# Optimization experiments

Measured on AMD Instinct MI355X. Metric: run time of the kernel, lower is better.

Reference implementation:

```python
import jax, jax.numpy as jnp
import numpy as np

HIDDEN = 1024
N_HEADS = 16
HEAD_DIM = HIDDEN // N_HEADS


def _rope_tables(seq_len, dim, dtype):
    inv_freq = 1.0 / (10000.0 ** (jnp.arange(0, dim, 2, dtype=jnp.float32) / dim))
    t = jnp.arange(seq_len, dtype=jnp.float32)
    freqs = jnp.einsum('i,j->ij', t, inv_freq)          # [S, dim/2]
    emb = jnp.concatenate([freqs, freqs], axis=-1)       # [S, dim]
    cos = jnp.cos(emb)[None, :, None, :].astype(dtype)   # [1, S, 1, dim]
    sin = jnp.sin(emb)[None, :, None, :].astype(dtype)
    return cos, sin


def _rotate_half(x):
    x1, x2 = x[..., : x.shape[-1] // 2], x[..., x.shape[-1] // 2 :]
    return jnp.concatenate([-x2, x1], axis=-1)


def setup_inputs() -> dict:
    key = jax.random.key(0)
    ks = jax.random.split(key, 9)
    s = 1.0 / np.sqrt(HIDDEN)
    return {
        'x': jax.random.normal(ks[0], (2, 2048, HIDDEN), dtype=jnp.float32),
        'q_w': jax.random.uniform(ks[1], (HIDDEN, HIDDEN), jnp.float32, -s, s),
        'q_b': jax.random.uniform(ks[2], (HIDDEN,), jnp.float32, -s, s),
        'k_w': jax.random.uniform(ks[3], (HIDDEN, HIDDEN), jnp.float32, -s, s),
        'k_b': jax.random.uniform(ks[4], (HIDDEN,), jnp.float32, -s, s),
        'v_w': jax.random.uniform(ks[5], (HIDDEN, HIDDEN), jnp.float32, -s, s),
        'v_b': jax.random.uniform(ks[6], (HIDDEN,), jnp.float32, -s, s),
        'o_w': jax.random.uniform(ks[7], (HIDDEN, HIDDEN), jnp.float32, -s, s),
        'o_b': jax.random.uniform(ks[8], (HIDDEN,), jnp.float32, -s, s),
    }


def reference(x, q_w, q_b, k_w, k_b, v_w, v_b, o_w, o_b):
    B, S, _ = x.shape
    scale = HEAD_DIM ** -0.5
    # projections (torch Linear: x @ W.T + b)
    q = (x @ q_w.T + q_b).reshape(B, S, N_HEADS, HEAD_DIM)
    k = (x @ k_w.T + k_b).reshape(B, S, N_HEADS, HEAD_DIM)
    v = (x @ v_w.T + v_b).reshape(B, S, N_HEADS, HEAD_DIM)
    # RoPE
    cos, sin = _rope_tables(S, HEAD_DIM, x.dtype)
    q = q * cos + _rotate_half(q) * sin
    k = k * cos + _rotate_half(k) * sin
    # attention: [B, H, S, S]
    scores = jnp.einsum('bqhd,bkhd->bhqk', q, k) * scale
    attn = jax.nn.softmax(scores, axis=-1)
    out = jnp.einsum('bhqk,bkhd->bqhd', attn, v).reshape(B, S, HIDDEN)
    return out @ o_w.T + o_b
```

## Files before the change

kernel.cpp:

```cpp
#include <hip/hip_runtime.h>
#include <hip/hip_bf16.h>


#define SEQ    2048
#define BATCH  2
#define NHEADS 16
#define HDIM   64
#define HID    1024
#define NTOK   (BATCH*SEQ)

typedef __bf16 bf16x8 __attribute__((ext_vector_type(8)));
typedef float  f32x4  __attribute__((ext_vector_type(4)));
typedef unsigned short u16x8 __attribute__((ext_vector_type(8)));

__device__ __forceinline__ unsigned short bfc(float x) {
  return __builtin_bit_cast(unsigned short, (__bf16)x);
}
#define EXP2(x) __builtin_amdgcn_exp2f(x)

__device__ __forceinline__ void gload16(const void* gptr, void* ldsptr) {
  typedef __attribute__((address_space(3))) unsigned int as3_uint;
  typedef const __attribute__((address_space(1))) unsigned int as1_uint;
  __builtin_amdgcn_global_load_lds(
      (as1_uint*)(unsigned long long)gptr,
      (as3_uint*)(unsigned int)(unsigned long long)ldsptr,
      16, 0, 0);
}

__device__ __forceinline__ void cvt8(const float* __restrict__ s,
                                     unsigned short* __restrict__ d, int i) {
  float4 a = *reinterpret_cast<const float4*>(s + i);
  float4 b = *reinterpret_cast<const float4*>(s + i + 4);
  u16x8 o;
  o[0] = bfc(a.x); o[1] = bfc(a.y); o[2] = bfc(a.z); o[3] = bfc(a.w);
  o[4] = bfc(b.x); o[5] = bfc(b.y); o[6] = bfc(b.z); o[7] = bfc(b.w);
  *reinterpret_cast<u16x8*>(d + i) = o;
}

__global__ __launch_bounds__(256) void prep(
    const float* __restrict__ x,
    const float* __restrict__ qw, const float* __restrict__ kw,
    const float* __restrict__ vw, const float* __restrict__ ow,
    unsigned short* __restrict__ xb,
    unsigned short* __restrict__ wqb, unsigned short* __restrict__ wkb,
    unsigned short* __restrict__ wvb, unsigned short* __restrict__ wob,
    float* __restrict__ ct, float* __restrict__ st)
{
  const int XN = NTOK * HID / 8;
  const int WN = HID * HID / 8;
  int tid = blockIdx.x * 256 + threadIdx.x;
  if (tid < XN) {
    cvt8(x, xb, tid * 8);
  } else if (tid < XN + 4 * WN) {
    int r = tid - XN;
    int which = r >> 17;
    int i = (r & (WN - 1)) * 8;
    const float* s = (which == 0) ? qw : (which == 1) ? kw : (which == 2) ? vw : ow;
    unsigned short* d = (which == 0) ? wqb : (which == 1) ? wkb : (which == 2) ? wvb : wob;
    cvt8(s, d, i);
  } else {
    int idx = tid - (XN + 4 * WN);
    if (idx < SEQ * 32) {
      int p = idx >> 5, j = idx & 31;
      float inv = powf(10000.0f, -(float)(2 * j) * (1.0f / 64.0f));
      float a = (float)p * inv;
      ct[idx] = cosf(a);
      st[idx] = sinf(a);
    }
  }
}

__global__ __launch_bounds__(256) void gemm_qkv(
    const unsigned short* __restrict__ X,
    const unsigned short* __restrict__ Wq, const unsigned short* __restrict__ Wk,
    const unsigned short* __restrict__ Wv,
    const float* __restrict__ bq, const float* __restrict__ bk, const float* __restrict__ bv,
    const float* __restrict__ ct, const float* __restrict__ st,
    unsigned short* __restrict__ Qo, unsigned short* __restrict__ Ko,
    unsigned short* __restrict__ VTo)
{
  __shared__ unsigned short LSH[24576];
  const int z = blockIdx.z;
  const unsigned short* W = (z == 0) ? Wq : (z == 1) ? Wk : Wv;
  const float* bias = (z == 0) ? bq : (z == 1) ? bk : bv;
  const int tm = blockIdx.x, tn = blockIdx.y;
  const int t = threadIdx.x, w = t >> 6, l = t & 63;
  const int wm = w >> 1, wn = w & 1, g = l >> 4;

  f32x4 acc[4][4] = {};

  const int arow0 = tm * 128, brow0 = tn * 128;
  const int s0 = w * 2, s1 = w * 2 + 1;
  const int r0 = s0 * 16 + (l >> 2), r1 = s1 * 16 + (l >> 2);
  const int kc = (l & 3) * 8;

#define GSTAGE(buf, k0)                                                               \
  {                                                                                   \
    gload16(X + (long)(arow0 + r0) * HID + (k0) + kc, LSH + (buf) * 4096 + s0 * 512); \
    gload16(X + (long)(arow0 + r1) * HID + (k0) + kc, LSH + (buf) * 4096 + s1 * 512); \
    gload16(W + (long)(brow0 + r0) * HID + (k0) + kc, LSH + 12288 + (buf) * 4096 + s0 * 512); \
    gload16(W + (long)(brow0 + r1) * HID + (k0) + kc, LSH + 12288 + (buf) * 4096 + s1 * 512); \
  }

  GSTAGE(0, 0)
  GSTAGE(1, 32)
  asm volatile("s_waitcnt vmcnt(4)" ::: "memory");
  __builtin_amdgcn_s_barrier();
  int cur = 0, stg = 2;
  for (int k0 = 0; k0 < HID; k0 += 32) {
    if (k0 + 64 < HID) GSTAGE(stg, k0 + 64)
    bf16x8 af[4], bfr[4];
#pragma unroll
    for (int fm = 0; fm < 4; ++fm)
      af[fm] = *reinterpret_cast<const bf16x8*>(
          LSH + cur * 4096 + (wm * 64 + fm * 16 + (l & 15)) * 32 + g * 8);
#pragma unroll
    for (int fn = 0; fn < 4; ++fn)
      bfr[fn] = *reinterpret_cast<const bf16x8*>(
          LSH + 12288 + cur * 4096 + (wn * 64 + fn * 16 + (l & 15)) * 32 + g * 8);
    __builtin_amdgcn_s_setprio(1);
#pragma unroll
    for (int fm = 0; fm < 4; ++fm)
#pragma unroll
      for (int fn = 0; fn < 4; ++fn)
        acc[fm][fn] = __builtin_amdgcn_mfma_f32_16x16x32_bf16(af[fm], bfr[fn], acc[fm][fn], 0, 0, 0);
    __builtin_amdgcn_s_setprio(0);
    if (k0 + 64 < HID) {
      asm volatile("s_waitcnt vmcnt(4)" ::: "memory");
    } else {
      asm volatile("s_waitcnt vmcnt(0)" ::: "memory");
    }
    __builtin_amdgcn_s_barrier();
    cur = (cur == 2) ? 0 : cur + 1;
    stg = (stg == 2) ? 0 : stg + 1;
  }
#undef GSTAGE

  const int colb = brow0 + wn * 64;
  float bsv[4];
#pragma unroll
  for (int fn = 0; fn < 4; ++fn) bsv[fn] = bias[colb + fn * 16 + (l & 15)];

  if (z == 2) {
#pragma unroll
    for (int fm = 0; fm < 4; ++fm) {
      int tok = wm * 64 + fm * 16 + g * 4;
#pragma unroll
      for (int fn = 0; fn < 4; ++fn) {
        int col = wn * 64 + fn * 16 + (l & 15);
        unsigned int u0 = (unsigned int)bfc(acc[fm][fn][0] + bsv[fn]) |
                          ((unsigned int)bfc(acc[fm][fn][1] + bsv[fn]) << 16);
        unsigned int u1 = (unsigned int)bfc(acc[fm][fn][2] + bsv[fn]) |
                          ((unsigned int)bfc(acc[fm][fn][3] + bsv[fn]) << 16);
        uint2 uv; uv.x = u0; uv.y = u1;
        *reinterpret_cast<uint2*>(&LSH[col * 128 + (tok ^ ((col & 7) << 3))]) = uv;
      }
    }
    __syncthreads();
    const int bb = arow0 >> 11, stok = arow0 & (SEQ - 1);
#pragma unroll
    for (int p8 = 0; p8 < 8; ++p8) {
      int col = p8 * 16 + (t >> 4);
      int soff = (t & 15) * 8;
      uint4 v = *reinterpret_cast<const uint4*>(&LSH[col * 128 + (soff ^ ((col & 7) << 3))]);
      int hh = (brow0 + col) >> 6;
      int dd = col & 63;
      unsigned short* dst = VTo + ((long)(bb * NHEADS + hh) * HDIM + dd) * SEQ + stok + soff;
      *reinterpret_cast<uint4*>(dst) = v;
    }
    return;
  }

  unsigned short* Out = (z == 0) ? Qo : Ko;
  const int h = colb >> 6;
#pragma unroll
  for (int fm = 0; fm < 4; ++fm) {
#pragma unroll
    for (int r = 0; r < 4; ++r) {
      int grow = arow0 + wm * 64 + fm * 16 + g * 4 + r;
      int b = grow >> 11, sidx = grow & (SEQ - 1);
      unsigned short* ob = Out + ((long)(b * NHEADS + h) * SEQ + sidx) * HDIM;
#pragma unroll
      for (int fn2 = 0; fn2 < 2; ++fn2) {
        int d1 = fn2 * 16 + (l & 15);
        float v1 = acc[fm][fn2][r] + bsv[fn2];
        float v2 = acc[fm][fn2 + 2][r] + bsv[fn2 + 2];
        float c = ct[sidx * 32 + d1], sn = st[sidx * 32 + d1];
        float o1 = v1 * c - v2 * sn;
        float o2 = v2 * c + v1 * sn;
        if (z == 0) { o1 *= 0.18033688f; o2 *= 0.18033688f; }
        ob[d1] = bfc(o1);
        ob[d1 + 32] = bfc(o2);
      }
    }
  }
}

__global__ __launch_bounds__(256) void attn(
    const unsigned short* __restrict__ Qb,
    const unsigned short* __restrict__ Kb,
    const unsigned short* __restrict__ VTb,
    unsigned short* __restrict__ Ob)
{
  __shared__ unsigned short Kl[2][64 * 64];
  __shared__ unsigned short Vl[4][64 * 64];
  __shared__ unsigned short Pl[4][32 * 64];
  __shared__ unsigned short Vext[16 * 64];
  const int bh = blockIdx.x, qt = blockIdx.y;
  const int b = bh >> 4, h = bh & 15;
  const int t = threadIdx.x, w = t >> 6, l = t & 63;
  const long hb = (long)bh * SEQ * HDIM;
  const int g = l >> 4;
  const int swz = (l & 7) << 4;

  const int q0 = qt * 128 + w * 32;
  bf16x8 qf[2][2];
#pragma unroll
  for (int f = 0; f < 2; ++f)
#pragma unroll
    for (int ks = 0; ks < 2; ++ks)
      qf[f][ks] = *reinterpret_cast<const bf16x8*>(
          Qb + hb + (long)(q0 + f * 16 + (l & 15)) * HDIM + ks * 32 + g * 8);

  f32x4 oacc[2][4] = {};
  f32x4 oaccE[2] = {};
  const f32x4 FZERO = {0.f, 0.f, 0.f, 0.f};

  const int rowq = (l & 15) * 128;
  const int colx0 = (g * 16) ^ swz;
  const int colx1 = (64 + g * 16) ^ swz;
  char* const Pw = (char*)Pl + w * 4096;

  const int srow = l >> 3;
  const int scol = (((l & 7) * 16) ^ ((l >> 3) << 4)) >> 1;
  const unsigned short* kp0 = Kb + hb + (long)(w * 16 + srow) * HDIM + scol;
  const unsigned short* kp1 = kp0 + 8 * HDIM;
  const unsigned short* vp0 = VTb + hb + (long)(w * 16 + srow) * SEQ + scol;
  const unsigned short* vp1 = vp0 + 8 * SEQ;

#define STAGE(kbuf, vbuf)                                              \
  {                                                                    \
    gload16(kp0, (char*)Kl + (kbuf) * 8192 + w * 2048);                \
    gload16(kp1, (char*)Kl + (kbuf) * 8192 + w * 2048 + 1024);         \
    gload16(vp0, (char*)Vl + (vbuf) * 8192 + w * 2048);                \
    gload16(vp1, (char*)Vl + (vbuf) * 8192 + w * 2048 + 1024);         \
    kp0 += 64 * HDIM; kp1 += 64 * HDIM; vp0 += 64; vp1 += 64;          \
  }

#define QK(kbuf)                                                                  \
  _Pragma("unroll")                                                               \
  for (int fnK = 0; fnK < 4; ++fnK) {                                             \
    const char* kb_ = (char*)Kl + (kbuf) * 8192 + fnK * 2048 + rowq;              \
    bf16x8 kf0 = *reinterpret_cast<const bf16x8*>(kb_ + colx0);                   \
    bf16x8 kf1 = *reinterpret_cast<const bf16x8*>(kb_ + colx1);                   \
    sa[0][fnK] = __builtin_amdgcn_mfma_f32_16x16x32_bf16(kf0, qf[0][0], FZERO, 0, 0, 0); \
    sa[0][fnK] = __builtin_amdgcn_mfma_f32_16x16x32_bf16(kf1, qf[0][1], sa[0][fnK], 0, 0, 0); \
    sa[1][fnK] = __builtin_amdgcn_mfma_f32_16x16x32_bf16(kf0, qf[1][0], FZERO, 0, 0, 0); \
    sa[1][fnK] = __builtin_amdgcn_mfma_f32_16x16x32_bf16(kf1, qf[1][1], sa[1][fnK], 0, 0, 0); \
  }

#define PFREAD                                                                    \
  _Pragma("unroll")                                                               \
  for (int f = 0; f < 2; ++f) {                                                   \
    pf[f][0] = *reinterpret_cast<const bf16x8*>(Pw + f * 2048 + rowq + colx0);    \
    pf[f][1] = *reinterpret_cast<const bf16x8*>(Pw + f * 2048 + rowq + colx1);    \
  }

#define PVSTEP(vbuf)                                                              \
  _Pragma("unroll")                                                               \
  for (int fnD = 0; fnD < 4; ++fnD) {                                             \
    const char* vb_ = (char*)Vl + (vbuf) * 8192 + fnD * 2048 + rowq;              \
    bf16x8 vf0 = *reinterpret_cast<const bf16x8*>(vb_ + colx0);                   \
    bf16x8 vf1 = *reinterpret_cast<const bf16x8*>(vb_ + colx1);                   \
    oacc[0][fnD] = __builtin_amdgcn_mfma_f32_16x16x32_bf16(vf0, pf[0][0], oacc[0][fnD], 0, 0, 0); \
    oacc[0][fnD] = __builtin_amdgcn_mfma_f32_16x16x32_bf16(vf1, pf[0][1], oacc[0][fnD], 0, 0, 0); \
    oacc[1][fnD] = __builtin_amdgcn_mfma_f32_16x16x32_bf16(vf0, pf[1][0], oacc[1][fnD], 0, 0, 0); \
    oacc[1][fnD] = __builtin_amdgcn_mfma_f32_16x16x32_bf16(vf1, pf[1][1], oacc[1][fnD], 0, 0, 0); \
  }                                                                               \
  oaccE[0] = __builtin_amdgcn_mfma_f32_16x16x32_bf16(vxf0, pf[0][0], oaccE[0], 0, 0, 0); \
  oaccE[0] = __builtin_amdgcn_mfma_f32_16x16x32_bf16(vxf1, pf[0][1], oaccE[0], 0, 0, 0); \
  oaccE[1] = __builtin_amdgcn_mfma_f32_16x16x32_bf16(vxf0, pf[1][0], oaccE[1], 0, 0, 0); \
  oaccE[1] = __builtin_amdgcn_mfma_f32_16x16x32_bf16(vxf1, pf[1][1], oaccE[1], 0, 0, 0);

#define SOFTPACK                                                                  \
  _Pragma("unroll")                                                               \
  for (int f = 0; f < 2; ++f) {                                                   \
    _Pragma("unroll")                                                             \
    for (int fn = 0; fn < 4; ++fn)                                                \
      _Pragma("unroll")                                                           \
      for (int r = 0; r < 4; ++r) sa[f][fn][r] = EXP2(sa[f][fn][r]);              \
    char* pw_ = Pw + f * 2048 + rowq;                                             \
    _Pragma("unroll")                                                             \
    for (int fn = 0; fn < 4; ++fn) {                                              \
      unsigned int u0 = (unsigned int)bfc(sa[f][fn][0]) | ((unsigned int)bfc(sa[f][fn][1]) << 16); \
      unsigned int u1 = (unsigned int)bfc(sa[f][fn][2]) | ((unsigned int)bfc(sa[f][fn][3]) << 16); \
      uint2 uv; uv.x = u0; uv.y = u1;                                             \
      *reinterpret_cast<uint2*>(pw_ + ((fn * 32 + g * 8) ^ swz)) = uv;            \
    }                                                                             \
  }

#define ITER(KB, VR, VW)                                   \
  {                                                        \
    PFREAD                                                 \
    STAGE(KB ^ 1, VW)                                      \
    __builtin_amdgcn_s_setprio(1);                         \
    QK(KB)                                                 \
    PVSTEP(VR)                                             \
    __builtin_amdgcn_s_setprio(0);                         \
    SOFTPACK                                               \
    asm volatile("s_waitcnt vmcnt(0)" ::: "memory");       \
    __builtin_amdgcn_s_barrier();                          \
  }
#define ITER_NOSTAGE(KB, VR)                               \
  {                                                        \
    PFREAD                                                 \
    __builtin_amdgcn_s_setprio(1);                         \
    QK(KB)                                                 \
    PVSTEP(VR)                                             \
    __builtin_amdgcn_s_setprio(0);                         \
    SOFTPACK                                               \
    asm volatile("s_waitcnt vmcnt(0)" ::: "memory");       \
    __builtin_amdgcn_s_barrier();                          \
  }

  f32x4 sa[2][4];
  bf16x8 pf[2][2];

  {
    int i = t * 4;
#pragma unroll
    for (int j = 0; j < 4; ++j)
      Vext[i + j] = (i + j) < 64 ? (unsigned short)0x3F80 : (unsigned short)0;
  }

  STAGE(0, 0)
  asm volatile("s_waitcnt vmcnt(0)" ::: "memory");
  __builtin_amdgcn_s_barrier();

  const bf16x8 vxf0 = *reinterpret_cast<const bf16x8*>((char*)Vext + rowq + colx0);
  const bf16x8 vxf1 = *reinterpret_cast<const bf16x8*>((char*)Vext + rowq + colx1);

  STAGE(1, 1)
  __builtin_amdgcn_s_setprio(1);
  QK(0)
  __builtin_amdgcn_s_setprio(0);
  SOFTPACK
  asm volatile("s_waitcnt vmcnt(0)" ::: "memory");
  __builtin_amdgcn_s_barrier();

  for (int m = 0; m < 7; ++m) {
    ITER(1, 0, 2)
    ITER(0, 1, 3)
    ITER(1, 2, 0)
    ITER(0, 3, 1)
  }
  ITER(1, 0, 2)
  ITER(0, 1, 3)
  ITER_NOSTAGE(1, 2)

  PFREAD
  __builtin_amdgcn_s_setprio(1);
  PVSTEP(3)
  __builtin_amdgcn_s_setprio(0);

#undef STAGE
#undef QK
#undef PFREAD
#undef PVSTEP
#undef SOFTPACK
#undef ITER
#undef ITER_NOSTAGE

#pragma unroll
  for (int f = 0; f < 2; ++f) {
    float lr = __shfl(oaccE[f][0], l & 15);
    float inv = 1.0f / lr;
    int q = q0 + f * 16 + (l & 15);
    unsigned short* op = Ob + (long)(b * SEQ + q) * HID + h * HDIM;
#pragma unroll
    for (int fnD = 0; fnD < 4; ++fnD) {
      unsigned int lo = (unsigned int)bfc(oacc[f][fnD][0] * inv) |
                        ((unsigned int)bfc(oacc[f][fnD][1] * inv) << 16);
      unsigned int hi = (unsigned int)bfc(oacc[f][fnD][2] * inv) |
                        ((unsigned int)bfc(oacc[f][fnD][3] * inv) << 16);
      uint2 uv; uv.x = lo; uv.y = hi;
      *reinterpret_cast<uint2*>(op + fnD * 16 + g * 4) = uv;
    }
  }
}

__global__ __launch_bounds__(256) void gemm_o(
    const unsigned short* __restrict__ A,
    const unsigned short* __restrict__ W,
    const float* __restrict__ bias,
    float* __restrict__ Out)
{
  __shared__ unsigned short Al[3][128 * 32];
  __shared__ unsigned short Bl[3][64 * 32];
  const int tm = blockIdx.x, tn = blockIdx.y;
  const int t = threadIdx.x, w = t >> 6, l = t & 63;
  const int wm = w >> 1, wn = w & 1;

  f32x4 acc[4][2] = {};
  const int arow0 = tm * 128, brow0 = tn * 64;
  const int s0 = w * 2, s1 = w * 2 + 1;
  const int r0 = s0 * 16 + (l >> 2), r1 = s1 * 16 + (l >> 2);
  const int rb = w * 16 + (l >> 2);
  const int kc = (l & 3) * 8;

#define GSTAGE(buf, k0)                                                       \
  {                                                                           \
    gload16(A + (long)(arow0 + r0) * HID + (k0) + kc, Al[buf] + s0 * 512);    \
    gload16(A + (long)(arow0 + r1) * HID + (k0) + kc, Al[buf] + s1 * 512);    \
    gload16(W + (long)(brow0 + rb) * HID + (k0) + kc, Bl[buf] + w * 512);     \
  }

  GSTAGE(0, 0)
  GSTAGE(1, 32)
  asm volatile("s_waitcnt vmcnt(3)" ::: "memory");
  __builtin_amdgcn_s_barrier();
  int cur = 0, stg = 2;
  for (int k0 = 0; k0 < HID; k0 += 32) {
    if (k0 + 64 < HID) GSTAGE(stg, k0 + 64)
    bf16x8 af[4], bfr[2];
#pragma unroll
    for (int fm = 0; fm < 4; ++fm)
      af[fm] = *reinterpret_cast<const bf16x8*>(Al[cur] + (wm * 64 + fm * 16 + (l & 15)) * 32 + (l >> 4) * 8);
#pragma unroll
    for (int fn = 0; fn < 2; ++fn)
      bfr[fn] = *reinterpret_cast<const bf16x8*>(Bl[cur] + (wn * 32 + fn * 16 + (l & 15)) * 32 + (l >> 4) * 8);
    __builtin_amdgcn_s_setprio(1);
#pragma unroll
    for (int fm = 0; fm < 4; ++fm)
#pragma unroll
      for (int fn = 0; fn < 2; ++fn)
        acc[fm][fn] = __builtin_amdgcn_mfma_f32_16x16x32_bf16(af[fm], bfr[fn], acc[fm][fn], 0, 0, 0);
    __builtin_amdgcn_s_setprio(0);
    if (k0 + 64 < HID) {
      asm volatile("s_waitcnt vmcnt(3)" ::: "memory");
    } else {
      asm volatile("s_waitcnt vmcnt(0)" ::: "memory");
    }
    __builtin_amdgcn_s_barrier();
    cur = (cur == 2) ? 0 : cur + 1;
    stg = (stg == 2) ? 0 : stg + 1;
  }
#undef GSTAGE

  const int colb = brow0 + wn * 32;
  float bsv[2];
#pragma unroll
  for (int fn = 0; fn < 2; ++fn) bsv[fn] = bias[colb + fn * 16 + (l & 15)];
#pragma unroll
  for (int fm = 0; fm < 4; ++fm)
#pragma unroll
    for (int r = 0; r < 4; ++r) {
      int grow = arow0 + wm * 64 + fm * 16 + (l >> 4) * 4 + r;
#pragma unroll
      for (int fn = 0; fn < 2; ++fn)
        Out[(long)grow * HID + colb + fn * 16 + (l & 15)] = acc[fm][fn][r] + bsv[fn];
    }
}

extern "C" void kernel_launch(void* const* d_in, const int* in_sizes, int n_in,
                              void* d_out, int out_size, void* d_ws, size_t ws_size,
                              hipStream_t stream) {
  const float* x  = (const float*)d_in[0];
  const float* qw = (const float*)d_in[1];
  const float* qb = (const float*)d_in[2];
  const float* kw = (const float*)d_in[3];
  const float* kb = (const float*)d_in[4];
  const float* vw = (const float*)d_in[5];
  const float* vb = (const float*)d_in[6];
  const float* ow = (const float*)d_in[7];
  const float* ob = (const float*)d_in[8];
  float* out = (float*)d_out;

  char* p = (char*)d_ws;
  unsigned short* xb  = (unsigned short*)p; p += (size_t)NTOK * HID * 2;
  unsigned short* wqb = (unsigned short*)p; p += (size_t)HID * HID * 2;
  unsigned short* wkb = (unsigned short*)p; p += (size_t)HID * HID * 2;
  unsigned short* wvb = (unsigned short*)p; p += (size_t)HID * HID * 2;
  unsigned short* wob = (unsigned short*)p; p += (size_t)HID * HID * 2;
  unsigned short* Qb  = (unsigned short*)p; p += (size_t)NTOK * HID * 2;
  unsigned short* Kb  = (unsigned short*)p; p += (size_t)NTOK * HID * 2;
  unsigned short* VTb = (unsigned short*)p; p += (size_t)NTOK * HID * 2;
  float* ct = (float*)p; p += (size_t)SEQ * 32 * 4;
  float* st = (float*)p; p += (size_t)SEQ * 32 * 4;
  unsigned short* Ab  = xb;

  const int XN = NTOK * HID / 8, WN = HID * HID / 8;
  const int prep_threads = XN + 4 * WN + SEQ * 32;
  prep<<<dim3((prep_threads + 255) / 256), 256, 0, stream>>>(
      x, qw, kw, vw, ow, xb, wqb, wkb, wvb, wob, ct, st);

  gemm_qkv<<<dim3(NTOK / 128, HID / 128, 3), 256, 0, stream>>>(
      xb, wqb, wkb, wvb, qb, kb, vb, ct, st, Qb, Kb, VTb);

  attn<<<dim3(BATCH * NHEADS, SEQ / 128), 256, 0, stream>>>(Qb, Kb, VTb, Ab);

  gemm_o<<<dim3(NTOK / 128, HID / 64), 256, 0, stream>>>(Ab, wob, ob, out);
}
```

Measured before the change: 113.1 us.

## Switch attention to 32x32x16 MFMA and keep P in registers via permlane swap

The attention kernel now uses 32x32x16 bf16 MFMA tiles instead of 16x16x32, so each wave handles a 32-query tile with one accumulator per 32 columns. The exponentiated scores are repacked into the B-operand layout in registers with v_permlane32_swap, removing the LDS round trip for P and the shared Pl and Vext buffers. The row-sum MFMA now uses a register constant of ones. This cuts LDS traffic and instruction count, but raises register pressure and relies on the exact layout of permlane32_swap, which is available on gfx950.

```diff
diff --git a/kernel.cpp b/kernel.cpp
--- a/kernel.cpp
+++ b/kernel.cpp
@@ -11,12 +11,21 @@
 
 typedef __bf16 bf16x8 __attribute__((ext_vector_type(8)));
 typedef float  f32x4  __attribute__((ext_vector_type(4)));
+typedef float  f32x16 __attribute__((ext_vector_type(16)));
 typedef unsigned short u16x8 __attribute__((ext_vector_type(8)));
+typedef unsigned int   u32x4 __attribute__((ext_vector_type(4)));
 
 __device__ __forceinline__ unsigned short bfc(float x) {
   return __builtin_bit_cast(unsigned short, (__bf16)x);
 }
+__device__ __forceinline__ unsigned int pk(float lo, float hi) {
+  return (unsigned int)bfc(lo) | ((unsigned int)bfc(hi) << 16);
+}
+__device__ __forceinline__ void plswap(unsigned int& a, unsigned int& b) {
+  asm volatile("v_permlane32_swap_b32 %0, %1" : "+v"(a), "+v"(b));
+}
 #define EXP2(x) __builtin_amdgcn_exp2f(x)
+#define MFMA32(a, b, c) __builtin_amdgcn_mfma_f32_32x32x16_bf16(a, b, c, 0, 0, 0)
 
 __device__ __forceinline__ void gload16(const void* gptr, void* ldsptr) {
   typedef __attribute__((address_space(3))) unsigned int as3_uint;
@@ -204,32 +213,26 @@
 {
   __shared__ unsigned short Kl[2][64 * 64];
   __shared__ unsigned short Vl[4][64 * 64];
-  __shared__ unsigned short Pl[4][32 * 64];
-  __shared__ unsigned short Vext[16 * 64];
   const int bh = blockIdx.x, qt = blockIdx.y;
   const int b = bh >> 4, h = bh & 15;
   const int t = threadIdx.x, w = t >> 6, l = t & 63;
   const long hb = (long)bh * SEQ * HDIM;
-  const int g = l >> 4;
+  const int hh = l >> 5;
   const int swz = (l & 7) << 4;
 
   const int q0 = qt * 128 + w * 32;
-  bf16x8 qf[2][2];
-#pragma unroll
-  for (int f = 0; f < 2; ++f)
-#pragma unroll
-    for (int ks = 0; ks < 2; ++ks)
-      qf[f][ks] = *reinterpret_cast<const bf16x8*>(
-          Qb + hb + (long)(q0 + f * 16 + (l & 15)) * HDIM + ks * 32 + g * 8);
-
-  f32x4 oacc[2][4] = {};
-  f32x4 oaccE[2] = {};
-  const f32x4 FZERO = {0.f, 0.f, 0.f, 0.f};
-
-  const int rowq = (l & 15) * 128;
-  const int colx0 = (g * 16) ^ swz;
-  const int colx1 = (64 + g * 16) ^ swz;
-  char* const Pw = (char*)Pl + w * 4096;
+  bf16x8 qf[4];
+#pragma unroll
+  for (int dc = 0; dc < 4; ++dc)
+    qf[dc] = *reinterpret_cast<const bf16x8*>(
+        Qb + hb + (long)(q0 + (l & 31)) * HDIM + dc * 16 + hh * 8);
+
+  f32x16 oacc[2] = {};
+  f32x16 oaccE = {};
+  const f32x16 FZ16 = {};
+
+  u32x4 ou; ou[0] = 0x3F803F80u; ou[1] = 0x3F803F80u; ou[2] = 0x3F803F80u; ou[3] = 0x3F803F80u;
+  const bf16x8 ones8 = __builtin_bit_cast(bf16x8, ou);
 
   const int srow = l >> 3;
   const int scol = (((l & 7) * 16) ^ ((l >> 3) << 4)) >> 1;
@@ -249,143 +252,132 @@
 
 #define QK(kbuf)                                                                  \
   _Pragma("unroll")                                                               \
-  for (int fnK = 0; fnK < 4; ++fnK) {                                             \
-    const char* kb_ = (char*)Kl + (kbuf) * 8192 + fnK * 2048 + rowq;              \
-    bf16x8 kf0 = *reinterpret_cast<const bf16x8*>(kb_ + colx0);                   \
-    bf16x8 kf1 = *reinterpret_cast<const bf16x8*>(kb_ + colx1);                   \
-    sa[0][fnK] = __builtin_amdgcn_mfma_f32_16x16x32_bf16(kf0, qf[0][0], FZERO, 0, 0, 0); \
-    sa[0][fnK] = __builtin_amdgcn_mfma_f32_16x16x32_bf16(kf1, qf[0][1], sa[0][fnK], 0, 0, 0); \
-    sa[1][fnK] = __builtin_amdgcn_mfma_f32_16x16x32_bf16(kf0, qf[1][0], FZERO, 0, 0, 0); \
-    sa[1][fnK] = __builtin_amdgcn_mfma_f32_16x16x32_bf16(kf1, qf[1][1], sa[1][fnK], 0, 0, 0); \
-  }
-
-#define PFREAD                                                                    \
+  for (int blk = 0; blk < 2; ++blk) {                                             \
+    const char* kb_ = (char*)Kl + (kbuf) * 8192 + (32 * blk + (l & 31)) * 128;    \
+    bf16x8 kf0 = *reinterpret_cast<const bf16x8*>(kb_ + ((0 * 32 + hh * 16) ^ swz)); \
+    sa[blk] = MFMA32(kf0, qf[0], FZ16);                                           \
+    bf16x8 kf1 = *reinterpret_cast<const bf16x8*>(kb_ + ((1 * 32 + hh * 16) ^ swz)); \
+    sa[blk] = MFMA32(kf1, qf[1], sa[blk]);                                        \
+    bf16x8 kf2 = *reinterpret_cast<const bf16x8*>(kb_ + ((2 * 32 + hh * 16) ^ swz)); \
+    sa[blk] = MFMA32(kf2, qf[2], sa[blk]);                                        \
+    bf16x8 kf3 = *reinterpret_cast<const bf16x8*>(kb_ + ((3 * 32 + hh * 16) ^ swz)); \
+    sa[blk] = MFMA32(kf3, qf[3], sa[blk]);                                        \
+  }
+
+#define SOFTEXP                                                                   \
   _Pragma("unroll")                                                               \
-  for (int f = 0; f < 2; ++f) {                                                   \
-    pf[f][0] = *reinterpret_cast<const bf16x8*>(Pw + f * 2048 + rowq + colx0);    \
-    pf[f][1] = *reinterpret_cast<const bf16x8*>(Pw + f * 2048 + rowq + colx1);    \
-  }
-
-#define PVSTEP(vbuf)                                                              \
+  for (int blk = 0; blk < 2; ++blk)                                               \
+    _Pragma("unroll")                                                             \
+    for (int r = 0; r < 16; ++r) sa[blk][r] = EXP2(sa[blk][r]);
+
+#define PBUILD(PB)                                                                \
   _Pragma("unroll")                                                               \
-  for (int fnD = 0; fnD < 4; ++fnD) {                                             \
-    const char* vb_ = (char*)Vl + (vbuf) * 8192 + fnD * 2048 + rowq;              \
-    bf16x8 vf0 = *reinterpret_cast<const bf16x8*>(vb_ + colx0);                   \
-    bf16x8 vf1 = *reinterpret_cast<const bf16x8*>(vb_ + colx1);                   \
-    oacc[0][fnD] = __builtin_amdgcn_mfma_f32_16x16x32_bf16(vf0, pf[0][0], oacc[0][fnD], 0, 0, 0); \
-    oacc[0][fnD] = __builtin_amdgcn_mfma_f32_16x16x32_bf16(vf1, pf[0][1], oacc[0][fnD], 0, 0, 0); \
-    oacc[1][fnD] = __builtin_amdgcn_mfma_f32_16x16x32_bf16(vf0, pf[1][0], oacc[1][fnD], 0, 0, 0); \
-    oacc[1][fnD] = __builtin_amdgcn_mfma_f32_16x16x32_bf16(vf1, pf[1][1], oacc[1][fnD], 0, 0, 0); \
+  for (int blk = 0; blk < 2; ++blk) {                                             \
+    unsigned int w0a = pk(sa[blk][0], sa[blk][1]);                                \
+    unsigned int w1a = pk(sa[blk][2], sa[blk][3]);                                \
+    unsigned int w0b = pk(sa[blk][4], sa[blk][5]);                                \
+    unsigned int w1b = pk(sa[blk][6], sa[blk][7]);                                \
+    unsigned int w0c = pk(sa[blk][8], sa[blk][9]);                                \
+    unsigned int w1c = pk(sa[blk][10], sa[blk][11]);                              \
+    unsigned int w0d = pk(sa[blk][12], sa[blk][13]);                              \
+    unsigned int w1d = pk(sa[blk][14], sa[blk][15]);                              \
+    plswap(w0a, w0b); plswap(w1a, w1b);                                           \
+    plswap(w0c, w0d); plswap(w1c, w1d);                                           \
+    u32x4 f0; f0[0] = w0a; f0[1] = w1a; f0[2] = w0b; f0[3] = w1b;                 \
+    u32x4 f1; f1[0] = w0c; f1[1] = w1c; f1[2] = w0d; f1[3] = w1d;                 \
+    PB[2 * blk + 0] = __builtin_bit_cast(bf16x8, f0);                             \
+    PB[2 * blk + 1] = __builtin_bit_cast(bf16x8, f1);                             \
+  }
+
+#define PVSTEP(vbuf, PB)                                                          \
+  _Pragma("unroll")                                                               \
+  for (int db = 0; db < 2; ++db) {                                                \
+    const char* vb_ = (char*)Vl + (vbuf) * 8192 + (32 * db + (l & 31)) * 128;     \
+    _Pragma("unroll")                                                             \
+    for (int kc = 0; kc < 4; ++kc) {                                              \
+      bf16x8 vf = *reinterpret_cast<const bf16x8*>(vb_ + ((kc * 32 + hh * 16) ^ swz)); \
+      oacc[db] = MFMA32(vf, PB[kc], oacc[db]);                                    \
+    }                                                                             \
   }                                                                               \
-  oaccE[0] = __builtin_amdgcn_mfma_f32_16x16x32_bf16(vxf0, pf[0][0], oaccE[0], 0, 0, 0); \
-  oaccE[0] = __builtin_amdgcn_mfma_f32_16x16x32_bf16(vxf1, pf[0][1], oaccE[0], 0, 0, 0); \
-  oaccE[1] = __builtin_amdgcn_mfma_f32_16x16x32_bf16(vxf0, pf[1][0], oaccE[1], 0, 0, 0); \
-  oaccE[1] = __builtin_amdgcn_mfma_f32_16x16x32_bf16(vxf1, pf[1][1], oaccE[1], 0, 0, 0);
-
-#define SOFTPACK                                                                  \
   _Pragma("unroll")                                                               \
-  for (int f = 0; f < 2; ++f) {                                                   \
-    _Pragma("unroll")                                                             \
-    for (int fn = 0; fn < 4; ++fn)                                                \
-      _Pragma("unroll")                                                           \
-      for (int r = 0; r < 4; ++r) sa[f][fn][r] = EXP2(sa[f][fn][r]);              \
-    char* pw_ = Pw + f * 2048 + rowq;                                             \
-    _Pragma("unroll")                                                             \
-    for (int fn = 0; fn < 4; ++fn) {                                              \
-      unsigned int u0 = (unsigned int)bfc(sa[f][fn][0]) | ((unsigned int)bfc(sa[f][fn][1]) << 16); \
-      unsigned int u1 = (unsigned int)bfc(sa[f][fn][2]) | ((unsigned int)bfc(sa[f][fn][3]) << 16); \
-      uint2 uv; uv.x = u0; uv.y = u1;                                             \
-      *reinterpret_cast<uint2*>(pw_ + ((fn * 32 + g * 8) ^ swz)) = uv;            \
-    }                                                                             \
-  }
-
-#define ITER(KB, VR, VW)                                   \
+  for (int kc = 0; kc < 4; ++kc) oaccE = MFMA32(ones8, PB[kc], oaccE);
+
+#define ITER(KB, VR, VW, PPREV, PNXT)                      \
   {                                                        \
-    PFREAD                                                 \
     STAGE(KB ^ 1, VW)                                      \
     __builtin_amdgcn_s_setprio(1);                         \
     QK(KB)                                                 \
-    PVSTEP(VR)                                             \
+    PVSTEP(VR, PPREV)                                      \
     __builtin_amdgcn_s_setprio(0);                         \
-    SOFTPACK                                               \
+    SOFTEXP                                                \
+    PBUILD(PNXT)                                           \
     asm volatile("s_waitcnt vmcnt(0)" ::: "memory");       \
     __builtin_amdgcn_s_barrier();                          \
   }
-#define ITER_NOSTAGE(KB, VR)                               \
+#define ITER_NOSTAGE(KB, VR, PPREV, PNXT)                  \
   {                                                        \
-    PFREAD                                                 \
     __builtin_amdgcn_s_setprio(1);                         \
     QK(KB)                                                 \
-    PVSTEP(VR)                                             \
+    PVSTEP(VR, PPREV)                                      \
     __builtin_amdgcn_s_setprio(0);                         \
-    SOFTPACK                                               \
+    SOFTEXP                                                \
+    PBUILD(PNXT)                                           \
     asm volatile("s_waitcnt vmcnt(0)" ::: "memory");       \
     __builtin_amdgcn_s_barrier();                          \
   }
 
-  f32x4 sa[2][4];
-  bf16x8 pf[2][2];
-
-  {
-    int i = t * 4;
-#pragma unroll
-    for (int j = 0; j < 4; ++j)
-      Vext[i + j] = (i + j) < 64 ? (unsigned short)0x3F80 : (unsigned short)0;
-  }
+  f32x16 sa[2];
+  bf16x8 pBa[4], pBb[4];
 
   STAGE(0, 0)
   asm volatile("s_waitcnt vmcnt(0)" ::: "memory");
   __builtin_amdgcn_s_barrier();
-
-  const bf16x8 vxf0 = *reinterpret_cast<const bf16x8*>((char*)Vext + rowq + colx0);
-  const bf16x8 vxf1 = *reinterpret_cast<const bf16x8*>((char*)Vext + rowq + colx1);
 
   STAGE(1, 1)
   __builtin_amdgcn_s_setprio(1);
   QK(0)
   __builtin_amdgcn_s_setprio(0);
-  SOFTPACK
+  SOFTEXP
+  PBUILD(pBa)
   asm volatile("s_waitcnt vmcnt(0)" ::: "memory");
   __builtin_amdgcn_s_barrier();
 
   for (int m = 0; m < 7; ++m) {
-    ITER(1, 0, 2)
-    ITER(0, 1, 3)
-    ITER(1, 2, 0)
-    ITER(0, 3, 1)
-  }
-  ITER(1, 0, 2)
-  ITER(0, 1, 3)
-  ITER_NOSTAGE(1, 2)
-
-  PFREAD
+    ITER(1, 0, 2, pBa, pBb)
+    ITER(0, 1, 3, pBb, pBa)
+    ITER(1, 2, 0, pBa, pBb)
+    ITER(0, 3, 1, pBb, pBa)
+  }
+  ITER(1, 0, 2, pBa, pBb)
+  ITER(0, 1, 3, pBb, pBa)
+  ITER_NOSTAGE(1, 2, pBa, pBb)
+
   __builtin_amdgcn_s_setprio(1);
-  PVSTEP(3)
+  PVSTEP(3, pBb)
   __builtin_amdgcn_s_setprio(0);
 
 #undef STAGE
 #undef QK
-#undef PFREAD
+#undef SOFTEXP
+#undef PBUILD
 #undef PVSTEP
-#undef SOFTPACK
 #undef ITER
 #undef ITER_NOSTAGE
 
-#pragma unroll
-  for (int f = 0; f < 2; ++f) {
-    float lr = __shfl(oaccE[f][0], l & 15);
-    float inv = 1.0f / lr;
-    int q = q0 + f * 16 + (l & 15);
+  {
+    float inv = 1.0f / oaccE[0];
+    int q = q0 + (l & 31);
     unsigned short* op = Ob + (long)(b * SEQ + q) * HID + h * HDIM;
 #pragma unroll
-    for (int fnD = 0; fnD < 4; ++fnD) {
-      unsigned int lo = (unsigned int)bfc(oacc[f][fnD][0] * inv) |
-                        ((unsigned int)bfc(oacc[f][fnD][1] * inv) << 16);
-      unsigned int hi = (unsigned int)bfc(oacc[f][fnD][2] * inv) |
-                        ((unsigned int)bfc(oacc[f][fnD][3] * inv) << 16);
-      uint2 uv; uv.x = lo; uv.y = hi;
-      *reinterpret_cast<uint2*>(op + fnD * 16 + g * 4) = uv;
-    }
+    for (int db = 0; db < 2; ++db)
+#pragma unroll
+      for (int a = 0; a < 4; ++a) {
+        int d = 8 * a + 4 * hh + 32 * db;
+        unsigned int lo = pk(oacc[db][4 * a + 0] * inv, oacc[db][4 * a + 1] * inv);
+        unsigned int hi2 = pk(oacc[db][4 * a + 2] * inv, oacc[db][4 * a + 3] * inv);
+        uint2 uv; uv.x = lo; uv.y = hi2;
+        *reinterpret_cast<uint2*>(op + d) = uv;
+      }
   }
 }
 
```

Result: no change. 114.9 us (+1.5%).
